# Kernel tuning notes

Measured on AMD Instinct MI355X. Metric: run time of the kernel, lower is better.

The kernel has to match this reference:

```python
import jax, jax.numpy as jnp
import numpy as np

N = 100_000   # num nodes
E = 3_200_000 # num directed edges (before self-loops)
NEG_SLOPE = 0.2


def setup_inputs() -> dict:
    key = jax.random.key(0)
    ks = jax.random.split(key, 12)
    x = jax.random.normal(ks[0], (N, 2), jnp.float32)
    edge_index = jax.random.randint(ks[1], (2, E), 0, N, dtype=jnp.int32)
    # GATConv(2, 16): lin weight [2,16] (no bias), att_src/att_dst [16], out bias [16]
    W1 = jax.random.normal(ks[2], (2, 16), jnp.float32) * (1.0 / np.sqrt(2.0))
    a_src1 = jax.random.normal(ks[3], (16,), jnp.float32) * 0.25
    a_dst1 = jax.random.normal(ks[4], (16,), jnp.float32) * 0.25
    b1 = jnp.zeros((16,), jnp.float32)
    # GATConv(16, 64)
    W2 = jax.random.normal(ks[5], (16, 64), jnp.float32) * (1.0 / np.sqrt(16.0))
    a_src2 = jax.random.normal(ks[6], (64,), jnp.float32) * 0.125
    a_dst2 = jax.random.normal(ks[7], (64,), jnp.float32) * 0.125
    b2 = jnp.zeros((64,), jnp.float32)
    return {"x": x, "edge_index": edge_index,
            "W1": W1, "a_src1": a_src1, "a_dst1": a_dst1, "b1": b1,
            "W2": W2, "a_src2": a_src2, "a_dst2": a_dst2, "b2": b2}


def _gat_layer(x, src, dst, W, a_src, a_dst, b):
    # x: [N, Fin]; src/dst: [E'] (self-loops included). Single head, PyG GATConv math.
    h = x @ W                                        # [N, Fout]
    alpha_s = h @ a_src                              # [N]
    alpha_d = h @ a_dst                              # [N]
    e = jax.nn.leaky_relu(alpha_s[src] + alpha_d[dst], NEG_SLOPE)  # [E']
    # segment softmax over incoming edges of each dst node
    m = jax.ops.segment_max(e, dst, num_segments=N)
    m = jnp.where(jnp.isfinite(m), m, 0.0)           # nodes always have a self-loop, but be safe
    p = jnp.exp(e - m[dst])
    s = jax.ops.segment_sum(p, dst, num_segments=N)
    alpha = p / s[dst]                               # [E']
    out = jax.ops.segment_sum(alpha[:, None] * h[src], dst, num_segments=N)  # [N, Fout]
    return out + b


def reference(x, edge_index, W1, a_src1, a_dst1, b1, W2, a_src2, a_dst2, b2):
    # PyG GATConv adds self-loops by default
    loops = jnp.arange(N, dtype=edge_index.dtype)
    src = jnp.concatenate([edge_index[0], loops])
    dst = jnp.concatenate([edge_index[1], loops])
    h = jax.nn.relu(_gat_layer(x, src, dst, W1, a_src1, a_dst1, b1))
    h = jax.nn.relu(_gat_layer(h, src, dst, W2, a_src2, a_dst2, b2))
    return h
```

## Files before the change

kernel.cpp:

```cpp
#include <hip/hip_runtime.h>

#define NNODES 100000
#define NEDGES 3200000
#define ETOT   (NEDGES + NNODES)
#define NEG_SLOPE 0.2f
#define LOG2E 1.4426950408889634f

#define NPB 64
#define NBUCK ((NNODES + NPB - 1) / NPB)
#define NCHUNK 256
#define CHUNK_E ((ETOT + NCHUNK - 1) / NCHUNK)
#define M2 (NBUCK * NCHUNK)
#define NSB2 ((M2 + 511) / 512)

__device__ __forceinline__ unsigned short f2bf(float f) {
    unsigned u = __float_as_uint(f);
    u += 0x7FFFu + ((u >> 16) & 1u);
    return (unsigned short)(u >> 16);
}
__device__ __forceinline__ float bf2f(unsigned short h) {
    return __uint_as_float(((unsigned)h) << 16);
}

__device__ __forceinline__ void edge_sd(int e, const int* __restrict__ ei, int& s, int& d) {
    if (e < NEDGES) { s = ei[e]; d = ei[NEDGES + e]; }
    else            { s = e - NEDGES; d = s; }
}

__device__ __forceinline__ float lrelu(float v) {
    return v > 0.0f ? v : NEG_SLOPE * v;
}

__device__ __forceinline__ float edge_w(float z) {
    return __builtin_amdgcn_exp2f(lrelu(z));
}

__device__ __forceinline__ float bcast_lane(float v, int lane_imm) {
    return __int_as_float(__builtin_amdgcn_readlane(__float_as_int(v), lane_imm));
}

template<int CTRL>
__device__ __forceinline__ float dpp_mov(float v) {
    return __int_as_float(__builtin_amdgcn_mov_dpp(__float_as_int(v), CTRL, 0xF, 0xF, true));
}
template<int CTRL>
__device__ __forceinline__ float dpp_add(float v) { return v + dpp_mov<CTRL>(v); }
template<int IMM>
__device__ __forceinline__ float swz(float v) {
    return __int_as_float(__builtin_amdgcn_ds_swizzle(__float_as_int(v), IMM));
}
__device__ __forceinline__ float swz16_add(float v) { return v + swz<0x401F>(v); }
__device__ __forceinline__ float row16_sum(float v) {
    v = dpp_add<0x121>(v);
    v = dpp_add<0x122>(v);
    v = dpp_add<0x124>(v);
    v = dpp_add<0x128>(v);
    return v;
}
__device__ __forceinline__ float wave64_sum(float v) {
    v = row16_sum(v);
    v = swz16_add(v);
    v += __shfl_xor(v, 32);
    return v;
}


__global__ void chunk_hist(const int* __restrict__ ei, int* __restrict__ H) {
    __shared__ int h[NBUCK];
    int c = blockIdx.x;
    for (int i = threadIdx.x; i < NBUCK; i += blockDim.x) h[i] = 0;
    __syncthreads();
    int lo = c * CHUNK_E, hi = lo + CHUNK_E; if (hi > ETOT) hi = ETOT;
    for (int e = lo + threadIdx.x; e < hi; e += blockDim.x) {
        int d = (e < NEDGES) ? ei[NEDGES + e] : (e - NEDGES);
        atomicAdd(&h[d >> 6], 1);
    }
    __syncthreads();
    for (int i = threadIdx.x; i < NBUCK; i += blockDim.x) H[c * NBUCK + i] = h[i];
}

__global__ void cscan_local(const int* __restrict__ H, int* __restrict__ off,
                            int* __restrict__ bsum2) {
    __shared__ int arr[512];
    int blk = blockIdx.x, t = threadIdx.x;
    int i = blk * 512 + t;
    int v = (i < M2) ? H[(i & (NCHUNK - 1)) * NBUCK + (i >> 8)] : 0;
    arr[t] = v;
    __syncthreads();
    for (int o = 1; o < 512; o <<= 1) {
        int u = (t >= o) ? arr[t - o] : 0;
        __syncthreads();
        arr[t] += u;
        __syncthreads();
    }
    if (i < M2) off[i] = arr[t] - v;
    if (t == 511) bsum2[blk] = arr[t];
}

__global__ void cscan_bsum(const int* __restrict__ bsum2, int* __restrict__ boff2) {
    __shared__ int arr[1024];
    int t = threadIdx.x;
    int v = (t < NSB2) ? bsum2[t] : 0;
    arr[t] = v;
    __syncthreads();
    for (int o = 1; o < 1024; o <<= 1) {
        int u = (t >= o) ? arr[t - o] : 0;
        __syncthreads();
        arr[t] += u;
        __syncthreads();
    }
    if (t < NSB2) boff2[t] = arr[t] - v;
}

__global__ void cscan_add(int* __restrict__ off, const int* __restrict__ boff2) {
    int i = blockIdx.x * 512 + threadIdx.x;
    if (i < M2) off[i] += boff2[blockIdx.x];
}

__global__ __launch_bounds__(1024)
void chunk_scatter(const int* __restrict__ ei, const int* __restrict__ off,
                   const int* __restrict__ H, int* __restrict__ pairs) {
    __shared__ int plds[CHUNK_E];
    __shared__ unsigned short blds[CHUNK_E];
    __shared__ int sc[2048];
    __shared__ int lcur[NBUCK];
    __shared__ int gbase[NBUCK];
    int c = blockIdx.x, t = threadIdx.x;
    for (int b = t; b < 2048; b += 1024) sc[b] = (b < NBUCK) ? H[c * NBUCK + b] : 0;
    __syncthreads();
    for (int o = 1; o < 2048; o <<= 1) {
        int i1 = t + 1024;
        int v0 = (t >= o) ? sc[t - o] : 0;
        int v1 = (i1 >= o) ? sc[i1 - o] : 0;
        __syncthreads();
        sc[t] += v0; sc[i1] += v1;
        __syncthreads();
    }
    for (int b = t; b < NBUCK; b += 1024) {
        int excl = (b == 0) ? 0 : sc[b - 1];
        lcur[b]  = excl;
        gbase[b] = off[b * NCHUNK + c] - excl;
    }
    __syncthreads();
    int lo = c * CHUNK_E, hi = lo + CHUNK_E; if (hi > ETOT) hi = ETOT;
    int n = hi - lo;
    for (int e = lo + t; e < hi; e += 1024) {
        int s, d; edge_sd(e, ei, s, d);
        int b = d >> 6;
        int slot = atomicAdd(&lcur[b], 1);
        plds[slot] = ((d & 63) << 17) | s;
        blds[slot] = (unsigned short)b;
    }
    __syncthreads();
    for (int i = t; i < n; i += 1024)
        pairs[gbase[blds[i]] + i] = plds[i];
}

__global__ void fine_sort2(const int* __restrict__ off, const int* __restrict__ pairs,
                           int* __restrict__ row_start, int* __restrict__ csr_src) {
    __shared__ int arr[NPB];
    __shared__ int cur[NPB];
    int b = blockIdx.x;
    int t = threadIdx.x;
    int base = off[b * NCHUNK];
    int bend = (b == NBUCK - 1) ? ETOT : off[(b + 1) * NCHUNK];
    if (t < NPB) arr[t] = 0;
    __syncthreads();
    for (int i = base + t; i < bend; i += blockDim.x)
        atomicAdd(&arr[pairs[i] >> 17], 1);
    __syncthreads();
    int v = (t < NPB) ? arr[t] : 0;
    __syncthreads();
    for (int o = 1; o < NPB; o <<= 1) {
        int u = (t < NPB && t >= o) ? arr[t - o] : 0;
        __syncthreads();
        if (t < NPB) arr[t] += u;
        __syncthreads();
    }
    if (t < NPB) {
        int node = b * NPB + t;
        int start = base + arr[t] - v;
        cur[t] = start;
        if (node < NNODES) row_start[node] = start;
    }
    if (b == NBUCK - 1 && t == 0) row_start[NNODES] = ETOT;
    __syncthreads();
    for (int i = base + t; i < bend; i += blockDim.x) {
        int p = pairs[i];
        int slot = atomicAdd(&cur[p >> 17], 1);
        csr_src[slot] = p & 0x1FFFF;
    }
}

__global__ void prep(const float* __restrict__ W1, const float* __restrict__ as1,
                     const float* __restrict__ ad1, const float* __restrict__ W2,
                     const float* __restrict__ as2, const float* __restrict__ ad2,
                     float* __restrict__ cvec) {
    int t = threadIdx.x;
    if (t < 2) {
        float s = 0.f, d = 0.f;
        for (int f = 0; f < 16; ++f) { s += W1[t * 16 + f] * as1[f]; d += W1[t * 16 + f] * ad1[f]; }
        cvec[t] = s * LOG2E; cvec[2 + t] = d * LOG2E;
    }
    if (t < 16) {
        float s = 0.f, d = 0.f;
        for (int f = 0; f < 64; ++f) { s += W2[t * 64 + f] * as2[f]; d += W2[t * 64 + f] * ad2[f]; }
        cvec[4 + t] = s * LOG2E; cvec[20 + t] = d * LOG2E;
    }
}

__global__ void alpha1(const float* __restrict__ x, const float* __restrict__ cvec,
                       float4* __restrict__ nrec1, float* __restrict__ ad_) {
    int n = blockIdx.x * blockDim.x + threadIdx.x;
    if (n >= NNODES) return;
    float2 xv = ((const float2*)x)[n];
    float as = xv.x * cvec[0] + xv.y * cvec[1];
    ad_[n] = xv.x * cvec[2] + xv.y * cvec[3];
    nrec1[n] = make_float4(xv.x, xv.y, as, 0.f);
}

__global__ void agg_l1(const int* __restrict__ row_start, const int* __restrict__ csr_src,
                       const float4* __restrict__ nrec1, const float* __restrict__ ad_,
                       const float* __restrict__ W1, const float* __restrict__ b1,
                       const float* __restrict__ cvec,
                       float* __restrict__ nrec2, float* __restrict__ ad2_) {
    int wave = threadIdx.x >> 6, lane = threadIdx.x & 63;
    int node = blockIdx.x * 4 + wave;
    int base = row_start[node], end = row_start[node + 1];
    float adv = ad_[node];
    float a0 = 0.f, a1 = 0.f, ss = 0.f;
    for (int i = base + lane; i < end; i += 64) {
        int sj = csr_src[i];
        float4 r = nrec1[sj];
        float w = edge_w(r.z + adv);
        ss += w;
        a0 += w * r.x;
        a1 += w * r.y;
    }
    a0 = wave64_sum(a0); a1 = wave64_sum(a1); ss = wave64_sum(ss);
    int f = lane & 15;
    float v = (a0 * W1[f] + a1 * W1[16 + f]) / ss + b1[f];
    float vr = v > 0.f ? v : 0.f;
    unsigned short* grow = (unsigned short*)(nrec2 + (size_t)node * 16);
    if (lane < 16) grow[lane] = f2bf(vr);
    float s2 = vr * cvec[4 + f];
    float d2 = vr * cvec[20 + f];
    s2 = row16_sum(s2); d2 = row16_sum(d2);
    if (lane == 0) {
        nrec2[(size_t)node * 16 + 8] = s2;
        ad2_[node] = d2;
    }
}

__global__ void agg_l2(const int* __restrict__ row_start, const int* __restrict__ csr_src,
                       const float* __restrict__ nrec2, const float* __restrict__ ad_,
                       const float* __restrict__ W2, const float* __restrict__ b2,
                       float* __restrict__ out) {
    int wave = threadIdx.x >> 6, lane = threadIdx.x & 63;
    int node = blockIdx.x * 4 + wave;
    int base = row_start[node], end = row_start[node + 1];
    float adv = ad_[node];
    float acc[16];
#pragma unroll
    for (int k = 0; k < 16; ++k) acc[k] = 0.f;
    float ss = 0.f;
    for (int i = base + lane; i < end; i += 64) {
        int sj = csr_src[i];
        const float* recf = nrec2 + (size_t)sj * 16;
        const uint4* rec4 = (const uint4*)recf;
        uint4 u0 = rec4[0], u1 = rec4[1];
        float as2v = recf[8];
        float w = edge_w(as2v + adv);
        ss += w;
        unsigned uu[8] = {u0.x, u0.y, u0.z, u0.w, u1.x, u1.y, u1.z, u1.w};
#pragma unroll
        for (int j = 0; j < 8; ++j) {
            acc[2 * j]     += w * __uint_as_float(uu[j] << 16);
            acc[2 * j + 1] += w * __uint_as_float(uu[j] & 0xFFFF0000u);
        }
    }
#pragma unroll
    for (int j = 0; j < 8; ++j) {
        float keep = (lane & 1) ? acc[2 * j + 1] : acc[2 * j];
        float send = (lane & 1) ? acc[2 * j]     : acc[2 * j + 1];
        acc[j] = keep + dpp_mov<0xB1>(send);
    }
#pragma unroll
    for (int j = 0; j < 4; ++j) {
        float keep = (lane & 2) ? acc[2 * j + 1] : acc[2 * j];
        float send = (lane & 2) ? acc[2 * j]     : acc[2 * j + 1];
        acc[j] = keep + dpp_mov<0x4E>(send);
    }
#pragma unroll
    for (int j = 0; j < 2; ++j) {
        float keep = (lane & 4) ? acc[2 * j + 1] : acc[2 * j];
        float send = (lane & 4) ? acc[2 * j]     : acc[2 * j + 1];
        acc[j] = keep + swz<0x101F>(send);
    }
    float r;
    {
        float keep = (lane & 8) ? acc[1] : acc[0];
        float send = (lane & 8) ? acc[0] : acc[1];
        r = keep + swz<0x201F>(send);
    }
    r = swz16_add(r);
    r += __shfl_xor(r, 32);
    float st = wave64_sum(ss);
    float o = 0.f;
#pragma unroll
    for (int k = 0; k < 16; ++k)
        o += bcast_lane(r, k) * W2[k * 64 + lane];
    o = o / st + b2[lane];
    out[(size_t)node * 64 + lane] = o > 0.f ? o : 0.f;
}

extern "C" void kernel_launch(void* const* d_in, const int* in_sizes, int n_in,
                              void* d_out, int out_size, void* d_ws, size_t ws_size,
                              hipStream_t stream) {
    const float* x     = (const float*)d_in[0];
    const int*   ei    = (const int*)  d_in[1];
    const float* W1    = (const float*)d_in[2];
    const float* as1w  = (const float*)d_in[3];
    const float* ad1w  = (const float*)d_in[4];
    const float* b1    = (const float*)d_in[5];
    const float* W2    = (const float*)d_in[6];
    const float* as2w  = (const float*)d_in[7];
    const float* ad2w  = (const float*)d_in[8];
    const float* b2    = (const float*)d_in[9];
    float* out = (float*)d_out;

    int* row_start = (int*)d_ws;
    int* csr_src   = row_start + (NNODES + 4);
    float* nrec2   = (float*)(csr_src + ETOT);
    float* adb     = nrec2 + (size_t)NNODES * 16;
    float* ad2b    = adb + NNODES;
    float* cvec    = ad2b + NNODES;
    int* pairs     = (int*)(cvec + 64);
    int* H         = pairs + ETOT;
    int* off       = H + M2;
    int* bsum2     = off + M2;
    int* boff2     = bsum2 + 1024;
    float4* nrec1  = (float4*)(boff2 + 1024);

    const int B = 256;
    const int NB = (NNODES + B - 1) / B;

    chunk_hist<<<NCHUNK, 1024, 0, stream>>>(ei, H);
    cscan_local<<<NSB2, 512, 0, stream>>>(H, off, bsum2);
    cscan_bsum<<<1, 1024, 0, stream>>>(bsum2, boff2);
    cscan_add<<<NSB2, 512, 0, stream>>>(off, boff2);
    chunk_scatter<<<NCHUNK, 1024, 0, stream>>>(ei, off, H, pairs);
    fine_sort2<<<NBUCK, B, 0, stream>>>(off, pairs, row_start, csr_src);

    prep<<<1, 64, 0, stream>>>(W1, as1w, ad1w, W2, as2w, ad2w, cvec);

    alpha1<<<NB, B, 0, stream>>>(x, cvec, nrec1, adb);
    agg_l1<<<NNODES / 4, B, 0, stream>>>(row_start, csr_src, nrec1, adb, W1, b1,
                                         cvec, nrec2, ad2b);

    agg_l2<<<NNODES / 4, B, 0, stream>>>(row_start, csr_src, nrec2, ad2b, W2, b2, out);
}
```

Measured before the change: 231.4 us.

## Assign one half-wave per node in both GAT aggregation kernels

Both aggregation kernels now process two destination nodes per wavefront, 32 lanes each, instead of one node per 64-lane wave. With an average in-degree around 33, this is meant to cut idle lanes in the gather loop and halve the block count. The layer-2 epilogue now broadcasts the reduced features through shared memory rather than readlane, and each lane writes two outputs. The risk is that high-degree nodes need more loop iterations, and the shared-memory broadcast relies on wave-level lockstep without a barrier.

```diff
diff --git a/kernel.cpp b/kernel.cpp
--- a/kernel.cpp
+++ b/kernel.cpp
@@ -33,10 +33,6 @@
 
 __device__ __forceinline__ float edge_w(float z) {
     return __builtin_amdgcn_exp2f(lrelu(z));
-}
-
-__device__ __forceinline__ float bcast_lane(float v, int lane_imm) {
-    return __int_as_float(__builtin_amdgcn_readlane(__float_as_int(v), lane_imm));
 }
 
 template<int CTRL>
@@ -57,10 +53,9 @@
     v = dpp_add<0x128>(v);
     return v;
 }
-__device__ __forceinline__ float wave64_sum(float v) {
+__device__ __forceinline__ float half32_sum(float v) {
     v = row16_sum(v);
     v = swz16_add(v);
-    v += __shfl_xor(v, 32);
     return v;
 }
 
@@ -224,12 +219,14 @@
                        const float* __restrict__ W1, const float* __restrict__ b1,
                        const float* __restrict__ cvec,
                        float* __restrict__ nrec2, float* __restrict__ ad2_) {
-    int wave = threadIdx.x >> 6, lane = threadIdx.x & 63;
-    int node = blockIdx.x * 4 + wave;
+    int wave = threadIdx.x >> 6;
+    int half = (threadIdx.x >> 5) & 1;
+    int hlane = threadIdx.x & 31;
+    int node = blockIdx.x * 8 + wave * 2 + half;
     int base = row_start[node], end = row_start[node + 1];
     float adv = ad_[node];
     float a0 = 0.f, a1 = 0.f, ss = 0.f;
-    for (int i = base + lane; i < end; i += 64) {
+    for (int i = base + hlane; i < end; i += 32) {
         int sj = csr_src[i];
         float4 r = nrec1[sj];
         float w = edge_w(r.z + adv);
@@ -237,16 +234,16 @@
         a0 += w * r.x;
         a1 += w * r.y;
     }
-    a0 = wave64_sum(a0); a1 = wave64_sum(a1); ss = wave64_sum(ss);
-    int f = lane & 15;
+    a0 = half32_sum(a0); a1 = half32_sum(a1); ss = half32_sum(ss);
+    int f = hlane & 15;
     float v = (a0 * W1[f] + a1 * W1[16 + f]) / ss + b1[f];
     float vr = v > 0.f ? v : 0.f;
     unsigned short* grow = (unsigned short*)(nrec2 + (size_t)node * 16);
-    if (lane < 16) grow[lane] = f2bf(vr);
+    if (hlane < 16) grow[hlane] = f2bf(vr);
     float s2 = vr * cvec[4 + f];
     float d2 = vr * cvec[20 + f];
     s2 = row16_sum(s2); d2 = row16_sum(d2);
-    if (lane == 0) {
+    if (hlane == 0) {
         nrec2[(size_t)node * 16 + 8] = s2;
         ad2_[node] = d2;
     }
@@ -256,15 +253,18 @@
                        const float* __restrict__ nrec2, const float* __restrict__ ad_,
                        const float* __restrict__ W2, const float* __restrict__ b2,
                        float* __restrict__ out) {
-    int wave = threadIdx.x >> 6, lane = threadIdx.x & 63;
-    int node = blockIdx.x * 4 + wave;
+    __shared__ float tot[4][2][16];
+    int wave = threadIdx.x >> 6;
+    int half = (threadIdx.x >> 5) & 1;
+    int hlane = threadIdx.x & 31;
+    int node = blockIdx.x * 8 + wave * 2 + half;
     int base = row_start[node], end = row_start[node + 1];
     float adv = ad_[node];
     float acc[16];
 #pragma unroll
     for (int k = 0; k < 16; ++k) acc[k] = 0.f;
     float ss = 0.f;
-    for (int i = base + lane; i < end; i += 64) {
+    for (int i = base + hlane; i < end; i += 32) {
         int sj = csr_src[i];
         const float* recf = nrec2 + (size_t)sj * 16;
         const uint4* rec4 = (const uint4*)recf;
@@ -281,37 +281,43 @@
     }
 #pragma unroll
     for (int j = 0; j < 8; ++j) {
-        float keep = (lane & 1) ? acc[2 * j + 1] : acc[2 * j];
-        float send = (lane & 1) ? acc[2 * j]     : acc[2 * j + 1];
+        float keep = (hlane & 1) ? acc[2 * j + 1] : acc[2 * j];
+        float send = (hlane & 1) ? acc[2 * j]     : acc[2 * j + 1];
         acc[j] = keep + dpp_mov<0xB1>(send);
     }
 #pragma unroll
     for (int j = 0; j < 4; ++j) {
-        float keep = (lane & 2) ? acc[2 * j + 1] : acc[2 * j];
-        float send = (lane & 2) ? acc[2 * j]     : acc[2 * j + 1];
+        float keep = (hlane & 2) ? acc[2 * j + 1] : acc[2 * j];
+        float send = (hlane & 2) ? acc[2 * j]     : acc[2 * j + 1];
         acc[j] = keep + dpp_mov<0x4E>(send);
     }
 #pragma unroll
     for (int j = 0; j < 2; ++j) {
-        float keep = (lane & 4) ? acc[2 * j + 1] : acc[2 * j];
-        float send = (lane & 4) ? acc[2 * j]     : acc[2 * j + 1];
+        float keep = (hlane & 4) ? acc[2 * j + 1] : acc[2 * j];
+        float send = (hlane & 4) ? acc[2 * j]     : acc[2 * j + 1];
         acc[j] = keep + swz<0x101F>(send);
     }
     float r;
     {
-        float keep = (lane & 8) ? acc[1] : acc[0];
-        float send = (lane & 8) ? acc[0] : acc[1];
+        float keep = (hlane & 8) ? acc[1] : acc[0];
+        float send = (hlane & 8) ? acc[0] : acc[1];
         r = keep + swz<0x201F>(send);
     }
     r = swz16_add(r);
-    r += __shfl_xor(r, 32);
-    float st = wave64_sum(ss);
-    float o = 0.f;
-#pragma unroll
-    for (int k = 0; k < 16; ++k)
-        o += bcast_lane(r, k) * W2[k * 64 + lane];
-    o = o / st + b2[lane];
-    out[(size_t)node * 64 + lane] = o > 0.f ? o : 0.f;
+    float st = half32_sum(ss);
+    if (hlane < 16) tot[wave][half][hlane] = r;
+    float o0 = 0.f, o1 = 0.f;
+#pragma unroll
+    for (int k = 0; k < 16; ++k) {
+        float t = tot[wave][half][k];
+        o0 += t * W2[k * 64 + hlane];
+        o1 += t * W2[k * 64 + 32 + hlane];
+    }
+    float inv = 1.0f / st;
+    o0 = o0 * inv + b2[hlane];
+    o1 = o1 * inv + b2[32 + hlane];
+    out[(size_t)node * 64 + hlane]      = o0 > 0.f ? o0 : 0.f;
+    out[(size_t)node * 64 + 32 + hlane] = o1 > 0.f ? o1 : 0.f;
 }
 
 extern "C" void kernel_launch(void* const* d_in, const int* in_sizes, int n_in,
@@ -355,8 +361,8 @@
     prep<<<1, 64, 0, stream>>>(W1, as1w, ad1w, W2, as2w, ad2w, cvec);
 
     alpha1<<<NB, B, 0, stream>>>(x, cvec, nrec1, adb);
-    agg_l1<<<NNODES / 4, B, 0, stream>>>(row_start, csr_src, nrec1, adb, W1, b1,
+    agg_l1<<<NNODES / 8, B, 0, stream>>>(row_start, csr_src, nrec1, adb, W1, b1,
                                          cvec, nrec2, ad2b);
 
-    agg_l2<<<NNODES / 4, B, 0, stream>>>(row_start, csr_src, nrec2, ad2b, W2, b2, out);
-}
+    agg_l2<<<NNODES / 8, B, 0, stream>>>(row_start, csr_src, nrec2, ad2b, W2, b2, out);
+}
```

New measurement: 221.1 us. 4.4% less time.
